# Optimization experiments

Measured on AMD Instinct MI355X. Metric: run time of the kernel, lower is better.

The kernel has to match this reference:

```python
import jax, jax.numpy as jnp
import numpy as np

B, L = 512, 24576
HID = 10


def setup_inputs() -> dict:
    key = jax.random.key(0)
    ks = jax.random.split(key, 9)
    s = 0.1
    return {
        "x": jax.random.normal(ks[0], (B, L, 1), dtype=jnp.float32),
        "conv_w": jax.random.normal(ks[1], (1, 1, 3), dtype=jnp.float32) * s,
        "conv_b": jax.random.normal(ks[2], (1,), dtype=jnp.float32) * s,
        "w_ih": jax.random.normal(ks[3], (4 * HID, 1), dtype=jnp.float32) * s,
        "w_hh": jax.random.normal(ks[4], (4 * HID, HID), dtype=jnp.float32) * s,
        "b_ih": jax.random.normal(ks[5], (4 * HID,), dtype=jnp.float32) * s,
        "b_hh": jax.random.normal(ks[6], (4 * HID,), dtype=jnp.float32) * s,
        "mlp_w": jax.random.normal(ks[7], (3, HID), dtype=jnp.float32) * s,
        "mlp_b": jax.random.normal(ks[8], (3,), dtype=jnp.float32) * s,
    }


def reference(x, conv_w, conv_b, w_ih, w_hh, b_ih, b_hh, mlp_w, mlp_b):
    b, l, _ = x.shape
    lp = l // 3  # conv1d k=3 stride=3 -> non-overlapping windows
    seg = x[:, : lp * 3, 0].reshape(b, lp, 3)
    c = jnp.einsum('blk,k->bl', seg, conv_w[0, 0]) + conv_b[0]
    c = jax.nn.relu(c)  # (B, Lp)
    seq = c.T[:, :, None]  # (Lp, B, 1) seq-major, input_size=1
    # precompute input-side gate pre-activations for all timesteps
    xg = jnp.einsum('tbi,gi->tbg', seq, w_ih) + b_ih + b_hh  # (Lp, B, 4H)

    def step(carry, xg_t):
        h, cc = carry
        g = xg_t + h @ w_hh.T  # (B, 4H)
        i, f, gg, o = jnp.split(g, 4, axis=-1)  # torch gate order i,f,g,o
        i = jax.nn.sigmoid(i)
        f = jax.nn.sigmoid(f)
        gg = jnp.tanh(gg)
        o = jax.nn.sigmoid(o)
        cc = f * cc + i * gg
        h = o * jnp.tanh(cc)
        return (h, cc), None

    h0 = jnp.zeros((b, HID), dtype=x.dtype)
    (h_n, _), _ = jax.lax.scan(step, (h0, h0), xg)
    return h_n @ mlp_w.T + mlp_b  # (B, 3)
```

## Files before the change

kernel.cpp:

```cpp
#include <hip/hip_runtime.h>


#define DEV __device__ __forceinline__

typedef _Float16 half2v __attribute__((ext_vector_type(2)));

DEV float rl_f(float v, int lane) {
  return __int_as_float(__builtin_amdgcn_readlane(__float_as_int(v), lane));
}

DEV half2v rl_h2(half2v v, int lane) {
  int i = __builtin_amdgcn_readlane(__builtin_bit_cast(int, v), lane);
  return __builtin_bit_cast(half2v, i);
}

DEV half2v pkrtz(float a, float b) {
  return __builtin_bit_cast(half2v, __builtin_amdgcn_cvt_pkrtz(a, b));
}

template <int CTRL>
DEV float dpp_f(float v) {
#if __has_builtin(__builtin_amdgcn_mov_dpp)
  return __int_as_float(__builtin_amdgcn_mov_dpp(__float_as_int(v), CTRL, 0xF, 0xF, true));
#else
  return __int_as_float(__builtin_amdgcn_update_dpp(0, __float_as_int(v), CTRL, 0xF, 0xF, true));
#endif
}

DEV float fast_exp2(float x) {
#if __has_builtin(__builtin_amdgcn_exp2f)
  return __builtin_amdgcn_exp2f(x);
#else
  return __exp2f(x);
#endif
}

DEV float fast_rcp(float x) { return __builtin_amdgcn_rcpf(x); }

#if __has_builtin(__builtin_amdgcn_fdot2)
#define USE_FDOT2 1
#else
#define USE_FDOT2 0
#endif

constexpr int kB = 512;
constexpr int kL = 24576;
constexpr int kLp = 8192;
constexpr int kHid = 10;
constexpr int kChunk = 64;
constexpr int kNChunk = kLp / kChunk;

__global__ __launch_bounds__(256, 1) void lstm_fused(
    const float* __restrict__ x,
    const float* __restrict__ conv_w,
    const float* __restrict__ conv_b,
    const float* __restrict__ w_ih,
    const float* __restrict__ w_hh,
    const float* __restrict__ b_ih,
    const float* __restrict__ b_hh,
    const float* __restrict__ mlp_w,
    const float* __restrict__ mlp_b,
    float* __restrict__ out) {
  const int lane = threadIdx.x & 63;
  const int wave = threadIdx.x >> 6;
  const int b = blockIdx.x * 4 + wave;

  const int hid = lane >> 2;
  const int gt = lane & 3;
  const bool active = (lane < 40);
  const int r = active ? (gt * kHid + hid) : 0;

  const float cw0 = conv_w[0], cw1 = conv_w[1], cw2 = conv_w[2];
  const float cbv = conv_b[0];

  constexpr float kL2E = 1.4426950408889634f;
  const float smul = (gt == 2) ? (-2.0f * kL2E) : (-kL2E);

  const float wih = w_ih[r] * smul;
  const float bsum = (b_ih[r] + b_hh[r]) * smul;
  const float* wr = w_hh + r * kHid;
  const float w0s = wr[0] * smul, w1s = wr[1] * smul;
  const float w2s = wr[2] * smul, w3s = wr[3] * smul, w4s = wr[4] * smul;
  const float w5s = wr[5] * smul, w6s = wr[6] * smul, w7s = wr[7] * smul;
  const float w8s = wr[8] * smul, w9s = wr[9] * smul;

#if USE_FDOT2
  const half2v wp1 = pkrtz(w2s, w3s);
  const half2v wp2 = pkrtz(w4s, w5s);
  const half2v wp3 = pkrtz(w6s, w7s);
  const half2v wp4 = pkrtz(w8s, w9s);
#endif

  const float C4 = -4.0f * kL2E;
  const float C2 = 2.0f * kL2E;

  const float* xb = x + (size_t)b * kL;
  const int xoff = lane * 3;

  float x0 = xb[xoff + 0];
  float x1 = xb[xoff + 1];
  float x2 = xb[xoff + 2];

  float h = 0.0f;
  float cs = 0.0f;

  for (int ch = 0; ch < kNChunk; ++ch) {
    float ct = fmaf(x2, cw2, fmaf(x1, cw1, fmaf(x0, cw0, cbv)));
    ct = fmaxf(ct, 0.0f);

    if (ch + 1 < kNChunk) {
      const float* xn = xb + (size_t)(ch + 1) * (kChunk * 3) + xoff;
      x0 = xn[0];
      x1 = xn[1];
      x2 = xn[2];
    }

#pragma unroll 8
    for (int t = 0; t < kChunk; ++t) {
      const float ctv = rl_f(ct, t);
      const float xg = fmaf(ctv, wih, bsum);

      float pre;
#if USE_FDOT2
      const float h0 = rl_f(h, 0), h1 = rl_f(h, 4);
      const float hnb = dpp_f<0x104>(h);
      const half2v hpk = pkrtz(h, hnb);
      const half2v p23 = rl_h2(hpk, 8);
      const half2v p45 = rl_h2(hpk, 16);
      const half2v p67 = rl_h2(hpk, 24);
      const half2v p89 = rl_h2(hpk, 32);
      float pA = fmaf(h0, w0s, xg);
      pA = fmaf(h1, w1s, pA);
      pA = __builtin_amdgcn_fdot2(p23, wp1, pA, false);
      float pB = __builtin_amdgcn_fdot2(p45, wp2, 0.0f, false);
      pB = __builtin_amdgcn_fdot2(p67, wp3, pB, false);
      const float pC = __builtin_amdgcn_fdot2(p89, wp4, 0.0f, false);
      pre = (pA + pC) + pB;
#else
      const float h0 = rl_f(h, 0), h1 = rl_f(h, 4), h2 = rl_f(h, 8);
      const float h3 = rl_f(h, 12), h4 = rl_f(h, 16), h5 = rl_f(h, 20);
      const float h6 = rl_f(h, 24), h7 = rl_f(h, 28), h8 = rl_f(h, 32);
      const float h9 = rl_f(h, 36);
      float pA = fmaf(h0, w0s, xg);
      pA = fmaf(h1, w1s, pA);
      pA = fmaf(h2, w2s, pA);
      float pB = h3 * w3s;
      pB = fmaf(h4, w4s, pB);
      pB = fmaf(h5, w5s, pB);
      float pC = h6 * w6s;
      pC = fmaf(h7, w7s, pC);
      float pD = h8 * w8s;
      pD = fmaf(h9, w9s, pD);
      pre = (pA + pB) + (pC + pD);
#endif

      const float a = fast_rcp(1.0f + fast_exp2(pre));

      const float iv = dpp_f<0x00>(a);
      const float fv = dpp_f<0x55>(a);
      const float gv = dpp_f<0xAA>(a);
      const float ov = dpp_f<0xFF>(a);
      const float ov2 = ov + ov;

      const float ti = iv * C2;
      const float pig = iv * gv;
      const float csp = fmaf(fv, cs, ti);
      cs = fmaf(pig, C4, csp);

      const float s2 = fast_rcp(1.0f + fast_exp2(cs));
      h = fmaf(s2, ov2, -ov);
    }
  }

  if (lane < 3) {
    const float* mw = mlp_w + lane * kHid;
    float acc = mlp_b[lane];
    acc = fmaf(rl_f(h, 0), mw[0], acc);
    acc = fmaf(rl_f(h, 4), mw[1], acc);
    acc = fmaf(rl_f(h, 8), mw[2], acc);
    acc = fmaf(rl_f(h, 12), mw[3], acc);
    acc = fmaf(rl_f(h, 16), mw[4], acc);
    acc = fmaf(rl_f(h, 20), mw[5], acc);
    acc = fmaf(rl_f(h, 24), mw[6], acc);
    acc = fmaf(rl_f(h, 28), mw[7], acc);
    acc = fmaf(rl_f(h, 32), mw[8], acc);
    acc = fmaf(rl_f(h, 36), mw[9], acc);
    out[b * 3 + lane] = acc;
  }
}

extern "C" void kernel_launch(void* const* d_in, const int* in_sizes, int n_in,
                              void* d_out, int out_size, void* d_ws, size_t ws_size,
                              hipStream_t stream) {
  const float* x = (const float*)d_in[0];
  const float* conv_w = (const float*)d_in[1];
  const float* conv_b = (const float*)d_in[2];
  const float* w_ih = (const float*)d_in[3];
  const float* w_hh = (const float*)d_in[4];
  const float* b_ih = (const float*)d_in[5];
  const float* b_hh = (const float*)d_in[6];
  const float* mlp_w = (const float*)d_in[7];
  const float* mlp_b = (const float*)d_in[8];
  float* out = (float*)d_out;

  dim3 grid(kB / 4), block(256);
  hipLaunchKernelGGL(lstm_fused, grid, block, 0, stream, x, conv_w, conv_b,
                     w_ih, w_hh, b_ih, b_hh, mlp_w, mlp_b, out);
}
```

Baseline: 780.1 us.

## Interleave two independent batch recurrences per wave to hide serial latency

Each wave now runs the LSTM recurrence for two batch rows, interleaving their steps so that one chain's dependent instructions (readlane, exp, rcp, DPP) can fill the other chain's latency stalls. The launch changes from 128 blocks of 4 waves to 256 single-wave blocks, which halves the total wave count to 256 and spreads them across more CUs. The cost is more registers and instructions per wave and fewer waves to overlap, so the gain depends on whether per-wave ILP beats the wave-level interleaving the SIMD scheduler already provided.

```diff
diff --git a/kernel.cpp b/kernel.cpp
--- a/kernel.cpp
+++ b/kernel.cpp
@@ -50,7 +50,7 @@
 constexpr int kChunk = 64;
 constexpr int kNChunk = kLp / kChunk;
 
-__global__ __launch_bounds__(256, 1) void lstm_fused(
+__global__ __launch_bounds__(64, 1) void lstm_fused(
     const float* __restrict__ x,
     const float* __restrict__ conv_w,
     const float* __restrict__ conv_b,
@@ -62,8 +62,8 @@
     const float* __restrict__ mlp_b,
     float* __restrict__ out) {
   const int lane = threadIdx.x & 63;
-  const int wave = threadIdx.x >> 6;
-  const int b = blockIdx.x * 4 + wave;
+  const int bA = blockIdx.x * 2;
+  const int bB = bA + 1;
 
   const int hid = lane >> 2;
   const int gt = lane & 3;
@@ -94,98 +94,110 @@
   const float C4 = -4.0f * kL2E;
   const float C2 = 2.0f * kL2E;
 
-  const float* xb = x + (size_t)b * kL;
+  const float* xbA = x + (size_t)bA * kL;
+  const float* xbB = x + (size_t)bB * kL;
   const int xoff = lane * 3;
 
-  float x0 = xb[xoff + 0];
-  float x1 = xb[xoff + 1];
-  float x2 = xb[xoff + 2];
-
-  float h = 0.0f;
-  float cs = 0.0f;
+  float x0A = xbA[xoff + 0], x1A = xbA[xoff + 1], x2A = xbA[xoff + 2];
+  float x0B = xbB[xoff + 0], x1B = xbB[xoff + 1], x2B = xbB[xoff + 2];
+
+  float hA = 0.0f, csA = 0.0f;
+  float hB = 0.0f, csB = 0.0f;
+
+  auto step = [&](float& h, float& cs, float ct, int t) {
+    const float ctv = rl_f(ct, t);
+    const float xg = fmaf(ctv, wih, bsum);
+#if USE_FDOT2
+    const float h0 = rl_f(h, 0), h1 = rl_f(h, 4);
+    const float hnb = dpp_f<0x104>(h);
+    const half2v hpk = pkrtz(h, hnb);
+    const half2v p23 = rl_h2(hpk, 8);
+    const half2v p45 = rl_h2(hpk, 16);
+    const half2v p67 = rl_h2(hpk, 24);
+    const half2v p89 = rl_h2(hpk, 32);
+    float pA = fmaf(h0, w0s, xg);
+    pA = fmaf(h1, w1s, pA);
+    pA = __builtin_amdgcn_fdot2(p23, wp1, pA, false);
+    float pB = __builtin_amdgcn_fdot2(p45, wp2, 0.0f, false);
+    pB = __builtin_amdgcn_fdot2(p67, wp3, pB, false);
+    const float pC = __builtin_amdgcn_fdot2(p89, wp4, 0.0f, false);
+    const float pre = (pA + pC) + pB;
+#else
+    const float h0 = rl_f(h, 0), h1 = rl_f(h, 4), h2 = rl_f(h, 8);
+    const float h3 = rl_f(h, 12), h4 = rl_f(h, 16), h5 = rl_f(h, 20);
+    const float h6 = rl_f(h, 24), h7 = rl_f(h, 28), h8 = rl_f(h, 32);
+    const float h9 = rl_f(h, 36);
+    float pA = fmaf(h0, w0s, xg);
+    pA = fmaf(h1, w1s, pA);
+    pA = fmaf(h2, w2s, pA);
+    float pB = h3 * w3s;
+    pB = fmaf(h4, w4s, pB);
+    pB = fmaf(h5, w5s, pB);
+    float pC = h6 * w6s;
+    pC = fmaf(h7, w7s, pC);
+    float pD = h8 * w8s;
+    pD = fmaf(h9, w9s, pD);
+    const float pre = (pA + pB) + (pC + pD);
+#endif
+    const float a = fast_rcp(1.0f + fast_exp2(pre));
+    const float iv = dpp_f<0x00>(a);
+    const float fv = dpp_f<0x55>(a);
+    const float gv = dpp_f<0xAA>(a);
+    const float ov = dpp_f<0xFF>(a);
+    const float ov2 = ov + ov;
+    const float ti = iv * C2;
+    const float pig = iv * gv;
+    const float csp = fmaf(fv, cs, ti);
+    cs = fmaf(pig, C4, csp);
+    const float s2 = fast_rcp(1.0f + fast_exp2(cs));
+    h = fmaf(s2, ov2, -ov);
+  };
 
   for (int ch = 0; ch < kNChunk; ++ch) {
-    float ct = fmaf(x2, cw2, fmaf(x1, cw1, fmaf(x0, cw0, cbv)));
-    ct = fmaxf(ct, 0.0f);
+    float ctA = fmaf(x2A, cw2, fmaf(x1A, cw1, fmaf(x0A, cw0, cbv)));
+    ctA = fmaxf(ctA, 0.0f);
+    float ctB = fmaf(x2B, cw2, fmaf(x1B, cw1, fmaf(x0B, cw0, cbv)));
+    ctB = fmaxf(ctB, 0.0f);
 
     if (ch + 1 < kNChunk) {
-      const float* xn = xb + (size_t)(ch + 1) * (kChunk * 3) + xoff;
-      x0 = xn[0];
-      x1 = xn[1];
-      x2 = xn[2];
+      const float* xnA = xbA + (size_t)(ch + 1) * (kChunk * 3) + xoff;
+      const float* xnB = xbB + (size_t)(ch + 1) * (kChunk * 3) + xoff;
+      x0A = xnA[0]; x1A = xnA[1]; x2A = xnA[2];
+      x0B = xnB[0]; x1B = xnB[1]; x2B = xnB[2];
     }
 
-#pragma unroll 8
+#pragma unroll 4
     for (int t = 0; t < kChunk; ++t) {
-      const float ctv = rl_f(ct, t);
-      const float xg = fmaf(ctv, wih, bsum);
-
-      float pre;
-#if USE_FDOT2
-      const float h0 = rl_f(h, 0), h1 = rl_f(h, 4);
-      const float hnb = dpp_f<0x104>(h);
-      const half2v hpk = pkrtz(h, hnb);
-      const half2v p23 = rl_h2(hpk, 8);
-      const half2v p45 = rl_h2(hpk, 16);
-      const half2v p67 = rl_h2(hpk, 24);
-      const half2v p89 = rl_h2(hpk, 32);
-      float pA = fmaf(h0, w0s, xg);
-      pA = fmaf(h1, w1s, pA);
-      pA = __builtin_amdgcn_fdot2(p23, wp1, pA, false);
-      float pB = __builtin_amdgcn_fdot2(p45, wp2, 0.0f, false);
-      pB = __builtin_amdgcn_fdot2(p67, wp3, pB, false);
-      const float pC = __builtin_amdgcn_fdot2(p89, wp4, 0.0f, false);
-      pre = (pA + pC) + pB;
-#else
-      const float h0 = rl_f(h, 0), h1 = rl_f(h, 4), h2 = rl_f(h, 8);
-      const float h3 = rl_f(h, 12), h4 = rl_f(h, 16), h5 = rl_f(h, 20);
-      const float h6 = rl_f(h, 24), h7 = rl_f(h, 28), h8 = rl_f(h, 32);
-      const float h9 = rl_f(h, 36);
-      float pA = fmaf(h0, w0s, xg);
-      pA = fmaf(h1, w1s, pA);
-      pA = fmaf(h2, w2s, pA);
-      float pB = h3 * w3s;
-      pB = fmaf(h4, w4s, pB);
-      pB = fmaf(h5, w5s, pB);
-      float pC = h6 * w6s;
-      pC = fmaf(h7, w7s, pC);
-      float pD = h8 * w8s;
-      pD = fmaf(h9, w9s, pD);
-      pre = (pA + pB) + (pC + pD);
-#endif
-
-      const float a = fast_rcp(1.0f + fast_exp2(pre));
-
-      const float iv = dpp_f<0x00>(a);
-      const float fv = dpp_f<0x55>(a);
-      const float gv = dpp_f<0xAA>(a);
-      const float ov = dpp_f<0xFF>(a);
-      const float ov2 = ov + ov;
-
-      const float ti = iv * C2;
-      const float pig = iv * gv;
-      const float csp = fmaf(fv, cs, ti);
-      cs = fmaf(pig, C4, csp);
-
-      const float s2 = fast_rcp(1.0f + fast_exp2(cs));
-      h = fmaf(s2, ov2, -ov);
+      step(hA, csA, ctA, t);
+      step(hB, csB, ctB, t);
     }
   }
 
   if (lane < 3) {
     const float* mw = mlp_w + lane * kHid;
-    float acc = mlp_b[lane];
-    acc = fmaf(rl_f(h, 0), mw[0], acc);
-    acc = fmaf(rl_f(h, 4), mw[1], acc);
-    acc = fmaf(rl_f(h, 8), mw[2], acc);
-    acc = fmaf(rl_f(h, 12), mw[3], acc);
-    acc = fmaf(rl_f(h, 16), mw[4], acc);
-    acc = fmaf(rl_f(h, 20), mw[5], acc);
-    acc = fmaf(rl_f(h, 24), mw[6], acc);
-    acc = fmaf(rl_f(h, 28), mw[7], acc);
-    acc = fmaf(rl_f(h, 32), mw[8], acc);
-    acc = fmaf(rl_f(h, 36), mw[9], acc);
-    out[b * 3 + lane] = acc;
+    float accA = mlp_b[lane], accB = mlp_b[lane];
+    accA = fmaf(rl_f(hA, 0), mw[0], accA);
+    accB = fmaf(rl_f(hB, 0), mw[0], accB);
+    accA = fmaf(rl_f(hA, 4), mw[1], accA);
+    accB = fmaf(rl_f(hB, 4), mw[1], accB);
+    accA = fmaf(rl_f(hA, 8), mw[2], accA);
+    accB = fmaf(rl_f(hB, 8), mw[2], accB);
+    accA = fmaf(rl_f(hA, 12), mw[3], accA);
+    accB = fmaf(rl_f(hB, 12), mw[3], accB);
+    accA = fmaf(rl_f(hA, 16), mw[4], accA);
+    accB = fmaf(rl_f(hB, 16), mw[4], accB);
+    accA = fmaf(rl_f(hA, 20), mw[5], accA);
+    accB = fmaf(rl_f(hB, 20), mw[5], accB);
+    accA = fmaf(rl_f(hA, 24), mw[6], accA);
+    accB = fmaf(rl_f(hB, 24), mw[6], accB);
+    accA = fmaf(rl_f(hA, 28), mw[7], accA);
+    accB = fmaf(rl_f(hB, 28), mw[7], accB);
+    accA = fmaf(rl_f(hA, 32), mw[8], accA);
+    accB = fmaf(rl_f(hB, 32), mw[8], accB);
+    accA = fmaf(rl_f(hA, 36), mw[9], accA);
+    accB = fmaf(rl_f(hB, 36), mw[9], accB);
+    out[bA * 3 + lane] = accA;
+    out[bB * 3 + lane] = accB;
   }
 }
 
@@ -203,7 +215,7 @@
   const float* mlp_b = (const float*)d_in[8];
   float* out = (float*)d_out;
 
-  dim3 grid(kB / 4), block(256);
+  dim3 grid(kB / 2), block(64);
   hipLaunchKernelGGL(lstm_fused, grid, block, 0, stream, x, conv_w, conv_b,
                      w_ih, w_hh, b_ih, b_hh, mlp_w, mlp_b, out);
 }
```

Measured after the change: 1.353 ms. 1.73x slower.
